# Kernel tuning notes

Hardware: AMD Instinct MI355X
Metric: run time of the kernel (lower is better)

The kernel has to match this reference:

```python
import jax, jax.numpy as jnp
import numpy as np

B, T, E, D = 8, 2048, 1024, 128  # batch, seq (== block_size), n_embedding, head size


def setup_inputs() -> dict:
    key = jax.random.key(0)
    kx, kk, kq, kv = jax.random.split(key, 4)
    scale_w = E ** -0.5  # ~torch Linear init scale
    return {
        "x": jax.random.normal(kx, (B, T, E), dtype=jnp.float32),
        "Wk": jax.random.normal(kk, (E, D), dtype=jnp.float32) * scale_w,
        "Wq": jax.random.normal(kq, (E, D), dtype=jnp.float32) * scale_w,
        "Wv": jax.random.normal(kv, (E, D), dtype=jnp.float32) * scale_w,
    }


def reference(x, Wk, Wq, Wv):
    # Training path of SelfAttentionHead.forward (use_cache=False).
    k = x @ Wk  # [B,T,D]
    q = x @ Wq  # [B,T,D]
    v = x @ Wv  # [B,T,D]
    Tlen = x.shape[1]
    scores = jnp.einsum("btd,bsd->bts", q, k) * (Wk.shape[1] ** -0.5)  # [B,T,T]
    causal = jnp.tril(jnp.ones((Tlen, Tlen), dtype=bool))
    scores = jnp.where(causal, scores, jnp.float32(-jnp.inf))
    wei = jax.nn.softmax(scores, axis=-1)
    out = jnp.einsum("bts,bsd->btd", wei, v)  # [B,T,D]
    return out
```

## Files before the change

### kernel.cpp

```cpp
#include <hip/hip_runtime.h>
#include <hip/hip_bf16.h>
#include <stdint.h>

#define Bq 8
#define Tq 2048
#define Eq 1024
#define Dq 128
#define BLOCKS_PER_B 144
#define NBLK (Bq * BLOCKS_PER_B)

typedef __attribute__((ext_vector_type(8))) short short8;
typedef __attribute__((ext_vector_type(4))) float f32x4;

__device__ __forceinline__ unsigned short f2b(float f) {
  __hip_bfloat16 h = __float2bfloat16(f);
  return __builtin_bit_cast(unsigned short, h);
}
__device__ __forceinline__ float b2f(unsigned short u) {
  unsigned int x = ((unsigned int)u) << 16;
  return __builtin_bit_cast(float, x);
}
__device__ __forceinline__ void gload16(const void* g, void* l) {
  __builtin_amdgcn_global_load_lds(
      (const __attribute__((address_space(1))) unsigned int*)g,
      (__attribute__((address_space(3))) unsigned int*)l, 16, 0, 0);
}

__global__ __launch_bounds__(256) void prep_w_kernel(const float* __restrict__ wq,
                                                     const float* __restrict__ wk,
                                                     const float* __restrict__ wv,
                                                     unsigned short* __restrict__ wt) {
  __shared__ float tile[64][129];
  const int p  = blockIdx.x >> 4;
  const int e0 = (blockIdx.x & 15) * 64;
  const float* w = (p == 0) ? wq : (p == 1) ? wk : wv;
  const int tid = threadIdx.x;
#pragma unroll
  for (int i = 0; i < 32; ++i) {
    int idx = i * 256 + tid;
    int r = idx >> 7, c = idx & 127;
    tile[r][c] = w[(size_t)(e0 + r) * Dq + c];
  }
  __syncthreads();
  const int d = tid >> 1;
  const int es = (tid & 1) * 32;
  unsigned short* dst = wt + (size_t)p * Dq * Eq + (size_t)d * Eq + e0 + es;
#pragma unroll
  for (int c4 = 0; c4 < 8; ++c4) {
    ushort4 u;
    u.x = f2b(tile[es + c4 * 4 + 0][d]);
    u.y = f2b(tile[es + c4 * 4 + 1][d]);
    u.z = f2b(tile[es + c4 * 4 + 2][d]);
    u.w = f2b(tile[es + c4 * 4 + 3][d]);
    *reinterpret_cast<ushort4*>(dst + c4 * 4) = u;
  }
}

__global__ __launch_bounds__(256) void proj3_kernel(const float* __restrict__ x,
                                                    const unsigned short* __restrict__ wt,
                                                    unsigned short* __restrict__ qo,
                                                    unsigned short* __restrict__ ko,
                                                    unsigned short* __restrict__ vo) {
  __shared__ __align__(16) char As[2][4096];
  __shared__ __align__(16) char Bs[3][8192];

  const int bid = blockIdx.x;
  const int L   = (bid & 7) * 96 + (bid >> 3);
  const int rt  = L / 3;
  const int p   = L - rt * 3;
  const int row0 = rt * 64;

  const int tid  = threadIdx.x;
  const int lane = tid & 63;
  const int w    = tid >> 6;
  const int wm   = w >> 1, wn = w & 1;
  const int lrow = lane & 15;
  const int lgrp = lane >> 4;
  const char* wtbyte = (const char*)wt + (size_t)p * Dq * 2048;

  const int arow8 = tid >> 3;
  const int ac16  = tid & 7;
  const float* asrc = x + (size_t)(row0 + arow8) * Eq + ac16 * 4;

  auto BSTAGE = [&](int bufi, int ks) {
#pragma unroll
    for (int i = 0; i < 2; ++i) {
      int col = i * 64 + (tid >> 2);
      int off = (tid & 3) * 16;
      gload16(wtbyte + (size_t)col * 2048 + ks * 2 + (off ^ (((col >> 1) & 3) << 4)),
              Bs[bufi] + i * 4096 + w * 1024);
    }
  };
  auto ALOAD = [&](int ks, float4& r0, float4& r1) {
    r0 = *reinterpret_cast<const float4*>(asrc + ks);
    r1 = *reinterpret_cast<const float4*>(asrc + (size_t)32 * Eq + ks);
  };
  auto AWRITE = [&](int bufi, const float4& r0, const float4& r1) {
#pragma unroll
    for (int i = 0; i < 2; ++i) {
      const float4& f = i ? r1 : r0;
      int row = i * 32 + arow8;
      int byte = row * 64 + ((ac16 * 8) ^ (((row >> 1) & 3) << 4));
      ushort4 u;
      u.x = f2b(f.x); u.y = f2b(f.y); u.z = f2b(f.z); u.w = f2b(f.w);
      *reinterpret_cast<ushort4*>(As[bufi] + byte) = u;
    }
  };

  f32x4 acc[2][4];
#pragma unroll
  for (int m = 0; m < 2; ++m)
#pragma unroll
    for (int n = 0; n < 4; ++n) acc[m][n] = (f32x4){0.f, 0.f, 0.f, 0.f};

  float4 Pa0, Pa1, Pb0, Pb1;
  ALOAD(0, Pa0, Pa1);
  BSTAGE(0, 0);
  BSTAGE(1, 32);
  AWRITE(0, Pa0, Pa1);
  ALOAD(32, Pb0, Pb1);
  asm volatile("s_waitcnt lgkmcnt(0)" ::: "memory");
  __builtin_amdgcn_sched_barrier(0);
  __builtin_amdgcn_s_barrier();

  auto STEP = [&](int t, float4& W0, float4& W1, float4& L0, float4& L1) {
    if (t < 31) {
      asm volatile("s_waitcnt vmcnt(4)" ::: "memory");
    } else {
      asm volatile("s_waitcnt vmcnt(0)" ::: "memory");
    }
    __builtin_amdgcn_sched_barrier(0);
    __builtin_amdgcn_s_barrier();

    if (t < 30) {
      ALOAD((t + 2) * 32, L0, L1);
      BSTAGE((t + 2) % 3, (t + 2) * 32);
    }

    const char* Ab = As[t & 1];
    const char* Bb = Bs[t % 3];
    short8 af[2], bf_[4];
#pragma unroll
    for (int m = 0; m < 2; ++m) {
      int ar = wm * 32 + m * 16 + lrow;
      af[m] = *reinterpret_cast<const short8*>(Ab + ar * 64 + ((lgrp * 16) ^ (((ar >> 1) & 3) << 4)));
    }
#pragma unroll
    for (int n = 0; n < 4; ++n) {
      int bc = wn * 64 + n * 16 + lrow;
      bf_[n] = *reinterpret_cast<const short8*>(Bb + bc * 64 + ((lgrp * 16) ^ (((bc >> 1) & 3) << 4)));
    }
#pragma unroll
    for (int m = 0; m < 2; ++m)
#pragma unroll
      for (int n = 0; n < 4; ++n)
        acc[m][n] = __builtin_amdgcn_mfma_f32_16x16x32_bf16(af[m], bf_[n], acc[m][n], 0, 0, 0);

    if (t < 31) AWRITE((t + 1) & 1, W0, W1);
    asm volatile("s_waitcnt lgkmcnt(0)" ::: "memory");
  };

  for (int tt = 0; tt < 32; tt += 2) {
    STEP(tt,     Pb0, Pb1, Pa0, Pa1);
    STEP(tt + 1, Pa0, Pa1, Pb0, Pb1);
  }

  const int rg   = lgrp * 4;
  const int lcol = lrow;
  if (p < 2) {
    unsigned short* out = (p == 0) ? qo : ko;
#pragma unroll
    for (int m = 0; m < 2; ++m)
#pragma unroll
      for (int n = 0; n < 4; ++n)
#pragma unroll
        for (int r = 0; r < 4; ++r)
          out[(size_t)(row0 + wm * 32 + m * 16 + rg + r) * Dq + wn * 64 + n * 16 + lcol] =
              f2b(acc[m][n][r]);
  } else {
#pragma unroll
    for (int m = 0; m < 2; ++m)
#pragma unroll
      for (int n = 0; n < 4; ++n)
#pragma unroll
        for (int r = 0; r < 4; ++r) {
          int trow = row0 + wm * 32 + m * 16 + rg + r;
          int bb = trow >> 11;
          int t  = trow & (Tq - 1);
          vo[(size_t)bb * Dq * Tq + (size_t)(wn * 64 + n * 16 + lcol) * Tq + t] = f2b(acc[m][n][r]);
        }
  }
}

__global__ __launch_bounds__(256) void attn_kernel(const unsigned short* __restrict__ q,
                                                   const unsigned short* __restrict__ k,
                                                   const unsigned short* __restrict__ vT,
                                                   unsigned short* __restrict__ pO,
                                                   float* __restrict__ pl) {
  __shared__ __align__(16) char kbuf[16384];
  __shared__ __align__(16) char vbuf[16384];
  __shared__ __align__(16) unsigned short pbuf[4][1024];

  const int lane = threadIdx.x & 63;
  const int w    = threadIdx.x >> 6;
  const int bx   = blockIdx.x;
  const int b    = bx / BLOCKS_PER_B;
  int rm = bx - b * BLOCKS_PER_B;
  int g = 0, s = 0;
#pragma unroll
  for (int c = 1; c <= 8; ++c) {
    int cnt = 4 * c;
    if (rm < cnt) { g = 4 * (c - 1) + rm / c; s = rm % c; break; }
    rm -= cnt;
  }
  const int kv0      = 256 * s;
  const int kend_blk = min(kv0 + 256, 64 * g + 64);
  const int qb0      = 64 * g + 16 * w;
  const int kend_w   = qb0 + 16;

  const int lrow = lane & 15;
  const int lgrp = lane >> 4;
  const int lk8  = lgrp * 8;
  const float kscale = 0.08838834764831845f * 1.44269504088896340736f;
  const float M0 = 8.0f;
  unsigned short* pb = pbuf[w];
  const char* kgbase = (const char*)(k + (size_t)b * Tq * Dq);
  const char* vgbase = (const char*)(vT + (size_t)b * Dq * Tq);

  short8 ones;
#pragma unroll
  for (int j = 0; j < 8; ++j) ones[j] = (short)0x3F80;

  short8 kr[4], vr[4];
  auto LOADREGS = [&](int kvb) {
    const char* ks = kgbase + (size_t)kvb * 256;
#pragma unroll
    for (int i = 0; i < 4; ++i) {
      int yl = i * 4096 + w * 1024 + lane * 16;
      kr[i] = *reinterpret_cast<const short8*>(ks + yl);
    }
#pragma unroll
    for (int i = 0; i < 4; ++i) {
      int yl = i * 4096 + w * 1024 + lane * 16;
      int d  = yl >> 7;
      vr[i] = *reinterpret_cast<const short8*>(vgbase + (size_t)d * 4096 + kvb * 2 + (yl & 127));
    }
    __builtin_amdgcn_sched_barrier(0);
  };
  auto WRITEREGS = [&]() {
#pragma unroll
    for (int i = 0; i < 4; ++i) {
      int yl = i * 4096 + w * 1024 + lane * 16;
      *reinterpret_cast<short8*>(kbuf + (yl ^ ((((yl >> 8) & 7)) << 4))) = kr[i];
    }
#pragma unroll
    for (int i = 0; i < 4; ++i) {
      int yl = i * 4096 + w * 1024 + lane * 16;
      int d  = yl >> 7;
      int dst = (yl & ~127) | ((yl & 127) ^ ((d & 7) << 4));
      *reinterpret_cast<short8*>(vbuf + dst) = vr[i];
    }
  };

  short8 qf[4];
  const unsigned short* qrow = q + ((size_t)b * Tq + qb0 + lrow) * Dq;
#pragma unroll
  for (int kc = 0; kc < 4; ++kc)
    qf[kc] = *reinterpret_cast<const short8*>(qrow + kc * 32 + lk8);

  f32x4 o[8];
#pragma unroll
  for (int n = 0; n < 8; ++n) o[n] = (f32x4){0.f, 0.f, 0.f, 0.f};
  f32x4 ol = (f32x4){0.f, 0.f, 0.f, 0.f};
  const int rowg = qb0 + lgrp * 4;

  const int nsteps = (kend_blk - kv0) >> 6;
  LOADREGS(kv0);
  asm volatile("s_waitcnt vmcnt(0)" ::: "memory");
  WRITEREGS();
  asm volatile("s_waitcnt lgkmcnt(0)" ::: "memory");
  __builtin_amdgcn_sched_barrier(0);
  __builtin_amdgcn_s_barrier();

  for (int t = 0; t < nsteps; ++t) {
    const int kvb = kv0 + (t << 6);
    if (t + 1 < nsteps) LOADREGS(kvb + 64);

    if (kvb < kend_w) {
      f32x4 sf[4];
#pragma unroll
      for (int n = 0; n < 4; ++n) sf[n] = (f32x4){0.f, 0.f, 0.f, 0.f};
#pragma unroll
      for (int kc = 0; kc < 4; ++kc)
#pragma unroll
        for (int n = 0; n < 4; ++n) {
          int u = (n * 16 + lrow) * 256 + kc * 64 + lgrp * 16;
          short8 kf = *reinterpret_cast<const short8*>(kbuf + (u ^ ((lrow & 7) << 4)));
          sf[n] = __builtin_amdgcn_mfma_f32_16x16x32_bf16(qf[kc], kf, sf[n], 0, 0, 0);
        }

      const bool needmask = (kvb + 64 > qb0);
      float p[4][4];
#pragma unroll
      for (int n = 0; n < 4; ++n)
#pragma unroll
        for (int r = 0; r < 4; ++r) {
          float aa = sf[n][r] * kscale;
          if (needmask && (kvb + n * 16 + lrow > rowg + r)) aa = -1e30f;
          p[n][r] = exp2f(aa - M0);
        }

#pragma unroll
      for (int n = 0; n < 4; ++n)
#pragma unroll
        for (int r = 0; r < 4; ++r) {
          int row = lgrp * 4 + r;
          int byte = row * 128 + (n * 16 + lrow) * 2;
          byte ^= (row & 7) << 4;
          *reinterpret_cast<unsigned short*>(reinterpret_cast<char*>(pb) + byte) = f2b(p[n][r]);
        }
      asm volatile("s_waitcnt lgkmcnt(0)" ::: "memory");
      __builtin_amdgcn_sched_barrier(0);
      int rbyte0 = (lrow * 128 + lgrp * 16) ^ ((lrow & 7) << 4);
      int rbyte1 = (lrow * 128 + 64 + lgrp * 16) ^ ((lrow & 7) << 4);
      short8 pf0 = *reinterpret_cast<const short8*>(reinterpret_cast<char*>(pb) + rbyte0);
      short8 pf1 = *reinterpret_cast<const short8*>(reinterpret_cast<char*>(pb) + rbyte1);

#pragma unroll
      for (int n = 0; n < 8; ++n) {
        int u0 = (n * 16 + lrow) * 128 + lgrp * 16;
        short8 vf0 = *reinterpret_cast<const short8*>(vbuf + (u0 ^ ((lrow & 7) << 4)));
        short8 vf1 = *reinterpret_cast<const short8*>(vbuf + ((u0 + 64) ^ ((lrow & 7) << 4)));
        o[n] = __builtin_amdgcn_mfma_f32_16x16x32_bf16(pf0, vf0, o[n], 0, 0, 0);
        o[n] = __builtin_amdgcn_mfma_f32_16x16x32_bf16(pf1, vf1, o[n], 0, 0, 0);
      }
      ol = __builtin_amdgcn_mfma_f32_16x16x32_bf16(pf0, ones, ol, 0, 0, 0);
      ol = __builtin_amdgcn_mfma_f32_16x16x32_bf16(pf1, ones, ol, 0, 0, 0);
    }
    __builtin_amdgcn_s_barrier();
    if (t + 1 < nsteps) {
      asm volatile("s_waitcnt vmcnt(0)" ::: "memory");
      WRITEREGS();
      asm volatile("s_waitcnt lgkmcnt(0)" ::: "memory");
      __builtin_amdgcn_sched_barrier(0);
    }
    __builtin_amdgcn_s_barrier();
  }

  unsigned short* po = pO + (size_t)bx * (64 * 128) + (size_t)(16 * w) * 128;
#pragma unroll
  for (int n = 0; n < 8; ++n)
#pragma unroll
    for (int r = 0; r < 4; ++r)
      po[(size_t)(lgrp * 4 + r) * 128 + n * 16 + lrow] = f2b(o[n][r]);
  if (lrow == 0) {
#pragma unroll
    for (int r = 0; r < 4; ++r)
      pl[(size_t)bx * 64 + 16 * w + lgrp * 4 + r] = ol[r];
  }
}

__global__ __launch_bounds__(256) void combine_kernel(const unsigned short* __restrict__ pO,
                                                      const float* __restrict__ pl,
                                                      float* __restrict__ out) {
  const int tile = blockIdx.x;
  const int b = tile >> 5;
  const int g = tile & 31;
  const int qq = g >> 2, rr = g & 3;
  const int nseg = qq + 1;
  const int slot0 = b * BLOCKS_PER_B + g + 2 * qq * (qq - 1) + qq * rr;

  __shared__ float fac[64];
  const int t = threadIdx.x;
  if (t < 64) {
    float L = 0.f;
    for (int s = 0; s < nseg; ++s) L += pl[(size_t)(slot0 + s) * 64 + t];
    fac[t] = 1.0f / L;
  }
  __syncthreads();

#pragma unroll
  for (int pass = 0; pass < 8; ++pass) {
    int i4 = pass * 256 + t;
    int row = i4 >> 5;
    int c4 = i4 & 31;
    float4 acc = make_float4(0.f, 0.f, 0.f, 0.f);
    for (int s = 0; s < nseg; ++s) {
      const ushort4 u = reinterpret_cast<const ushort4*>(pO + (size_t)(slot0 + s) * 8192 + row * 128)[c4];
      acc.x += b2f(u.x);
      acc.y += b2f(u.y);
      acc.z += b2f(u.z);
      acc.w += b2f(u.w);
    }
    float f = fac[row];
    acc.x *= f; acc.y *= f; acc.z *= f; acc.w *= f;
    reinterpret_cast<float4*>(out + ((size_t)b * Tq + g * 64 + row) * Dq)[c4] = acc;
  }
}

extern "C" void kernel_launch(void* const* d_in, const int* in_sizes, int n_in,
                              void* d_out, int out_size, void* d_ws, size_t ws_size,
                              hipStream_t stream) {
  const float* x  = (const float*)d_in[0];
  const float* Wk = (const float*)d_in[1];
  const float* Wq = (const float*)d_in[2];
  const float* Wv = (const float*)d_in[3];
  float* out = (float*)d_out;

  unsigned short* wt = (unsigned short*)d_ws;
  unsigned short* qb = wt + (size_t)3 * Dq * Eq;
  unsigned short* kb = qb + (size_t)Bq * Tq * Dq;
  unsigned short* vb = kb + (size_t)Bq * Tq * Dq;
  unsigned short* pO = vb + (size_t)Bq * Tq * Dq;
  float* pl = (float*)(pO + (size_t)NBLK * 64 * 128);

  prep_w_kernel<<<48, 256, 0, stream>>>(Wq, Wk, Wv, wt);
  proj3_kernel<<<768, 256, 0, stream>>>(x, wt, qb, kb, vb);
  attn_kernel<<<NBLK, 256, 0, stream>>>(qb, kb, vb, pO, pl);
  combine_kernel<<<Bq * Tq / 64, 256, 0, stream>>>(pO, pl, out);
}
```

Before: 89.58 us.

## Enlarge projection tile to 256 rows with 512-thread blocks

```diff
diff --git a/kernel.cpp b/kernel.cpp
--- a/kernel.cpp
+++ b/kernel.cpp
@@ -56,76 +56,73 @@
   }
 }
 
-__global__ __launch_bounds__(256) void proj3_kernel(const float* __restrict__ x,
+__global__ __launch_bounds__(512) void proj3_kernel(const float* __restrict__ x,
                                                     const unsigned short* __restrict__ wt,
                                                     unsigned short* __restrict__ qo,
                                                     unsigned short* __restrict__ ko,
                                                     unsigned short* __restrict__ vo) {
-  __shared__ __align__(16) char As[2][4096];
+  __shared__ __align__(16) char As[2][16384];
   __shared__ __align__(16) char Bs[3][8192];
 
   const int bid = blockIdx.x;
-  const int L   = (bid & 7) * 96 + (bid >> 3);
+  const int L   = (bid & 7) * 24 + (bid >> 3);
   const int rt  = L / 3;
   const int p   = L - rt * 3;
-  const int row0 = rt * 64;
+  const int row0 = rt * 256;
 
   const int tid  = threadIdx.x;
   const int lane = tid & 63;
-  const int w    = tid >> 6;
-  const int wm   = w >> 1, wn = w & 1;
+  const int wid  = tid >> 6;
+  const int wm   = wid >> 1, wn = wid & 1;
   const int lrow = lane & 15;
   const int lgrp = lane >> 4;
   const char* wtbyte = (const char*)wt + (size_t)p * Dq * 2048;
 
-  const int arow8 = tid >> 3;
-  const int ac16  = tid & 7;
-  const float* asrc = x + (size_t)(row0 + arow8) * Eq + ac16 * 4;
+  const int arow = tid >> 3;
+  const int ac16 = tid & 7;
+  const float* asrc = x + (size_t)(row0 + arow) * Eq + ac16 * 4;
 
   auto BSTAGE = [&](int bufi, int ks) {
-#pragma unroll
-    for (int i = 0; i < 2; ++i) {
-      int col = i * 64 + (tid >> 2);
-      int off = (tid & 3) * 16;
-      gload16(wtbyte + (size_t)col * 2048 + ks * 2 + (off ^ (((col >> 1) & 3) << 4)),
-              Bs[bufi] + i * 4096 + w * 1024);
-    }
-  };
-  auto ALOAD = [&](int ks, float4& r0, float4& r1) {
-    r0 = *reinterpret_cast<const float4*>(asrc + ks);
-    r1 = *reinterpret_cast<const float4*>(asrc + (size_t)32 * Eq + ks);
-  };
-  auto AWRITE = [&](int bufi, const float4& r0, const float4& r1) {
-#pragma unroll
-    for (int i = 0; i < 2; ++i) {
-      const float4& f = i ? r1 : r0;
-      int row = i * 32 + arow8;
+    int col = tid >> 2;
+    int off = (tid & 3) * 16;
+    gload16(wtbyte + (size_t)col * 2048 + ks * 2 + (off ^ (((col >> 1) & 3) << 4)),
+            Bs[bufi] + tid * 16);
+  };
+  auto ALOAD = [&](f32x4* P, int ks) {
+#pragma unroll
+    for (int i = 0; i < 4; ++i)
+      P[i] = *reinterpret_cast<const f32x4*>(asrc + (size_t)i * 64 * Eq + ks);
+  };
+  auto AWRITE = [&](int bufi, const f32x4* P) {
+#pragma unroll
+    for (int i = 0; i < 4; ++i) {
+      int row = arow + i * 64;
       int byte = row * 64 + ((ac16 * 8) ^ (((row >> 1) & 3) << 4));
       ushort4 u;
-      u.x = f2b(f.x); u.y = f2b(f.y); u.z = f2b(f.z); u.w = f2b(f.w);
+      u.x = f2b(P[i][0]); u.y = f2b(P[i][1]); u.z = f2b(P[i][2]); u.w = f2b(P[i][3]);
       *reinterpret_cast<ushort4*>(As[bufi] + byte) = u;
     }
   };
 
-  f32x4 acc[2][4];
-#pragma unroll
-  for (int m = 0; m < 2; ++m)
+  f32x4 acc[4][4];
+#pragma unroll
+  for (int m = 0; m < 4; ++m)
 #pragma unroll
     for (int n = 0; n < 4; ++n) acc[m][n] = (f32x4){0.f, 0.f, 0.f, 0.f};
 
-  float4 Pa0, Pa1, Pb0, Pb1;
-  ALOAD(0, Pa0, Pa1);
+  f32x4 Pa[4], Pb[4];
+  ALOAD(Pa, 0);
   BSTAGE(0, 0);
+  AWRITE(0, Pa);
+  ALOAD(Pb, 32);
   BSTAGE(1, 32);
-  AWRITE(0, Pa0, Pa1);
-  ALOAD(32, Pb0, Pb1);
   asm volatile("s_waitcnt lgkmcnt(0)" ::: "memory");
   __builtin_amdgcn_sched_barrier(0);
   __builtin_amdgcn_s_barrier();
 
-  auto STEP = [&](int t, float4& W0, float4& W1, float4& L0, float4& L1) {
+  auto STEP = [&](int t, f32x4* W, f32x4* Ld) {
     if (t < 31) {
-      asm volatile("s_waitcnt vmcnt(4)" ::: "memory");
+      asm volatile("s_waitcnt vmcnt(5)" ::: "memory");
     } else {
       asm volatile("s_waitcnt vmcnt(0)" ::: "memory");
     }
@@ -133,16 +130,16 @@
     __builtin_amdgcn_s_barrier();
 
     if (t < 30) {
-      ALOAD((t + 2) * 32, L0, L1);
+      ALOAD(Ld, (t + 2) * 32);
       BSTAGE((t + 2) % 3, (t + 2) * 32);
     }
 
     const char* Ab = As[t & 1];
     const char* Bb = Bs[t % 3];
-    short8 af[2], bf_[4];
-#pragma unroll
-    for (int m = 0; m < 2; ++m) {
-      int ar = wm * 32 + m * 16 + lrow;
+    short8 af[4], bf_[4];
+#pragma unroll
+    for (int m = 0; m < 4; ++m) {
+      int ar = wm * 64 + m * 16 + lrow;
       af[m] = *reinterpret_cast<const short8*>(Ab + ar * 64 + ((lgrp * 16) ^ (((ar >> 1) & 3) << 4)));
     }
 #pragma unroll
@@ -151,18 +148,18 @@
       bf_[n] = *reinterpret_cast<const short8*>(Bb + bc * 64 + ((lgrp * 16) ^ (((bc >> 1) & 3) << 4)));
     }
 #pragma unroll
-    for (int m = 0; m < 2; ++m)
+    for (int m = 0; m < 4; ++m)
 #pragma unroll
       for (int n = 0; n < 4; ++n)
         acc[m][n] = __builtin_amdgcn_mfma_f32_16x16x32_bf16(af[m], bf_[n], acc[m][n], 0, 0, 0);
 
-    if (t < 31) AWRITE((t + 1) & 1, W0, W1);
+    if (t < 31) AWRITE((t + 1) & 1, W);
     asm volatile("s_waitcnt lgkmcnt(0)" ::: "memory");
   };
 
   for (int tt = 0; tt < 32; tt += 2) {
-    STEP(tt,     Pb0, Pb1, Pa0, Pa1);
-    STEP(tt + 1, Pa0, Pa1, Pb0, Pb1);
+    STEP(tt,     Pb, Pa);
+    STEP(tt + 1, Pa, Pb);
   }
 
   const int rg   = lgrp * 4;
@@ -170,21 +167,21 @@
   if (p < 2) {
     unsigned short* out = (p == 0) ? qo : ko;
 #pragma unroll
-    for (int m = 0; m < 2; ++m)
+    for (int m = 0; m < 4; ++m)
 #pragma unroll
       for (int n = 0; n < 4; ++n)
 #pragma unroll
         for (int r = 0; r < 4; ++r)
-          out[(size_t)(row0 + wm * 32 + m * 16 + rg + r) * Dq + wn * 64 + n * 16 + lcol] =
+          out[(size_t)(row0 + wm * 64 + m * 16 + rg + r) * Dq + wn * 64 + n * 16 + lcol] =
               f2b(acc[m][n][r]);
   } else {
 #pragma unroll
-    for (int m = 0; m < 2; ++m)
+    for (int m = 0; m < 4; ++m)
 #pragma unroll
       for (int n = 0; n < 4; ++n)
 #pragma unroll
         for (int r = 0; r < 4; ++r) {
-          int trow = row0 + wm * 32 + m * 16 + rg + r;
+          int trow = row0 + wm * 64 + m * 16 + rg + r;
           int bb = trow >> 11;
           int t  = trow & (Tq - 1);
           vo[(size_t)bb * Dq * Tq + (size_t)(wn * 64 + n * 16 + lcol) * Tq + t] = f2b(acc[m][n][r]);
@@ -415,7 +412,7 @@
   float* pl = (float*)(pO + (size_t)NBLK * 64 * 128);
 
   prep_w_kernel<<<48, 256, 0, stream>>>(Wq, Wk, Wv, wt);
-  proj3_kernel<<<768, 256, 0, stream>>>(x, wt, qb, kb, vb);
+  proj3_kernel<<<192, 512, 0, stream>>>(x, wt, qb, kb, vb);
   attn_kernel<<<NBLK, 256, 0, stream>>>(qb, kb, vb, pO, pl);
   combine_kernel<<<Bq * Tq / 64, 256, 0, stream>>>(pO, pl, out);
 }
```

Result: slower. 101.7 us (+13.5%).

## Double query rows per wave to reuse K/V tiles across 128-row blocks

Applied to the files above, without the earlier changes.

```diff
diff --git a/kernel.cpp b/kernel.cpp
--- a/kernel.cpp
+++ b/kernel.cpp
@@ -6,7 +6,7 @@
 #define Tq 2048
 #define Eq 1024
 #define Dq 128
-#define BLOCKS_PER_B 144
+#define BLOCKS_PER_B 72
 #define NBLK (Bq * BLOCKS_PER_B)
 
 typedef __attribute__((ext_vector_type(8))) short short8;
@@ -199,24 +199,24 @@
                                                    float* __restrict__ pl) {
   __shared__ __align__(16) char kbuf[16384];
   __shared__ __align__(16) char vbuf[16384];
-  __shared__ __align__(16) unsigned short pbuf[4][1024];
+  __shared__ __align__(16) unsigned short pbuf[4][2048];
 
   const int lane = threadIdx.x & 63;
   const int w    = threadIdx.x >> 6;
   const int bx   = blockIdx.x;
   const int b    = bx / BLOCKS_PER_B;
   int rm = bx - b * BLOCKS_PER_B;
-  int g = 0, s = 0;
+  int G = 0, s = 0;
 #pragma unroll
   for (int c = 1; c <= 8; ++c) {
-    int cnt = 4 * c;
-    if (rm < cnt) { g = 4 * (c - 1) + rm / c; s = rm % c; break; }
+    int cnt = 2 * c;
+    if (rm < cnt) { G = 2 * (c - 1) + rm / c; s = rm % c; break; }
     rm -= cnt;
   }
   const int kv0      = 256 * s;
-  const int kend_blk = min(kv0 + 256, 64 * g + 64);
-  const int qb0      = 64 * g + 16 * w;
-  const int kend_w   = qb0 + 16;
+  const int kend_blk = min(kv0 + 256, 128 * G + 128);
+  const int qb0      = 128 * G + 32 * w;
+  const int kend_w   = qb0 + 32;
 
   const int lrow = lane & 15;
   const int lgrp = lane >> 4;
@@ -262,17 +262,23 @@
     }
   };
 
-  short8 qf[4];
-  const unsigned short* qrow = q + ((size_t)b * Tq + qb0 + lrow) * Dq;
-#pragma unroll
-  for (int kc = 0; kc < 4; ++kc)
-    qf[kc] = *reinterpret_cast<const short8*>(qrow + kc * 32 + lk8);
-
-  f32x4 o[8];
-#pragma unroll
-  for (int n = 0; n < 8; ++n) o[n] = (f32x4){0.f, 0.f, 0.f, 0.f};
-  f32x4 ol = (f32x4){0.f, 0.f, 0.f, 0.f};
-  const int rowg = qb0 + lgrp * 4;
+  short8 qf[2][4];
+#pragma unroll
+  for (int rs = 0; rs < 2; ++rs) {
+    const unsigned short* qrow = q + ((size_t)b * Tq + qb0 + rs * 16 + lrow) * Dq;
+#pragma unroll
+    for (int kc = 0; kc < 4; ++kc)
+      qf[rs][kc] = *reinterpret_cast<const short8*>(qrow + kc * 32 + lk8);
+  }
+
+  f32x4 o[2][8];
+#pragma unroll
+  for (int rs = 0; rs < 2; ++rs)
+#pragma unroll
+    for (int n = 0; n < 8; ++n) o[rs][n] = (f32x4){0.f, 0.f, 0.f, 0.f};
+  f32x4 ol[2];
+  ol[0] = (f32x4){0.f, 0.f, 0.f, 0.f};
+  ol[1] = (f32x4){0.f, 0.f, 0.f, 0.f};
 
   const int nsteps = (kend_blk - kv0) >> 6;
   LOADREGS(kv0);
@@ -287,55 +293,64 @@
     if (t + 1 < nsteps) LOADREGS(kvb + 64);
 
     if (kvb < kend_w) {
-      f32x4 sf[4];
-#pragma unroll
-      for (int n = 0; n < 4; ++n) sf[n] = (f32x4){0.f, 0.f, 0.f, 0.f};
+      f32x4 sf[2][4];
+#pragma unroll
+      for (int rs = 0; rs < 2; ++rs)
+#pragma unroll
+        for (int n = 0; n < 4; ++n) sf[rs][n] = (f32x4){0.f, 0.f, 0.f, 0.f};
 #pragma unroll
       for (int kc = 0; kc < 4; ++kc)
 #pragma unroll
         for (int n = 0; n < 4; ++n) {
           int u = (n * 16 + lrow) * 256 + kc * 64 + lgrp * 16;
           short8 kf = *reinterpret_cast<const short8*>(kbuf + (u ^ ((lrow & 7) << 4)));
-          sf[n] = __builtin_amdgcn_mfma_f32_16x16x32_bf16(qf[kc], kf, sf[n], 0, 0, 0);
+          sf[0][n] = __builtin_amdgcn_mfma_f32_16x16x32_bf16(qf[0][kc], kf, sf[0][n], 0, 0, 0);
+          sf[1][n] = __builtin_amdgcn_mfma_f32_16x16x32_bf16(qf[1][kc], kf, sf[1][n], 0, 0, 0);
         }
 
-      const bool needmask = (kvb + 64 > qb0);
-      float p[4][4];
-#pragma unroll
-      for (int n = 0; n < 4; ++n)
-#pragma unroll
-        for (int r = 0; r < 4; ++r) {
-          float aa = sf[n][r] * kscale;
-          if (needmask && (kvb + n * 16 + lrow > rowg + r)) aa = -1e30f;
-          p[n][r] = exp2f(aa - M0);
-        }
-
-#pragma unroll
-      for (int n = 0; n < 4; ++n)
-#pragma unroll
-        for (int r = 0; r < 4; ++r) {
-          int row = lgrp * 4 + r;
-          int byte = row * 128 + (n * 16 + lrow) * 2;
-          byte ^= (row & 7) << 4;
-          *reinterpret_cast<unsigned short*>(reinterpret_cast<char*>(pb) + byte) = f2b(p[n][r]);
-        }
+#pragma unroll
+      for (int rs = 0; rs < 2; ++rs) {
+        const int rowg = qb0 + rs * 16 + lgrp * 4;
+        const bool needmask = (kvb + 64 > qb0 + rs * 16);
+#pragma unroll
+        for (int n = 0; n < 4; ++n)
+#pragma unroll
+          for (int r = 0; r < 4; ++r) {
+            float aa = sf[rs][n][r] * kscale;
+            if (needmask && (kvb + n * 16 + lrow > rowg + r)) aa = -1e30f;
+            float pv = exp2f(aa - M0);
+            int row = lgrp * 4 + r;
+            int byte = rs * 2048 + ((row * 128 + (n * 16 + lrow) * 2) ^ ((row & 7) << 4));
+            *reinterpret_cast<unsigned short*>(reinterpret_cast<char*>(pb) + byte) = f2b(pv);
+          }
+      }
       asm volatile("s_waitcnt lgkmcnt(0)" ::: "memory");
       __builtin_amdgcn_sched_barrier(0);
-      int rbyte0 = (lrow * 128 + lgrp * 16) ^ ((lrow & 7) << 4);
-      int rbyte1 = (lrow * 128 + 64 + lgrp * 16) ^ ((lrow & 7) << 4);
-      short8 pf0 = *reinterpret_cast<const short8*>(reinterpret_cast<char*>(pb) + rbyte0);
-      short8 pf1 = *reinterpret_cast<const short8*>(reinterpret_cast<char*>(pb) + rbyte1);
+      short8 pf[2][2];
+#pragma unroll
+      for (int rs = 0; rs < 2; ++rs) {
+        int rbyte0 = rs * 2048 + ((lrow * 128 + lgrp * 16) ^ ((lrow & 7) << 4));
+        int rbyte1 = rs * 2048 + ((lrow * 128 + 64 + lgrp * 16) ^ ((lrow & 7) << 4));
+        pf[rs][0] = *reinterpret_cast<const short8*>(reinterpret_cast<char*>(pb) + rbyte0);
+        pf[rs][1] = *reinterpret_cast<const short8*>(reinterpret_cast<char*>(pb) + rbyte1);
+      }
 
 #pragma unroll
       for (int n = 0; n < 8; ++n) {
         int u0 = (n * 16 + lrow) * 128 + lgrp * 16;
         short8 vf0 = *reinterpret_cast<const short8*>(vbuf + (u0 ^ ((lrow & 7) << 4)));
         short8 vf1 = *reinterpret_cast<const short8*>(vbuf + ((u0 + 64) ^ ((lrow & 7) << 4)));
-        o[n] = __builtin_amdgcn_mfma_f32_16x16x32_bf16(pf0, vf0, o[n], 0, 0, 0);
-        o[n] = __builtin_amdgcn_mfma_f32_16x16x32_bf16(pf1, vf1, o[n], 0, 0, 0);
+#pragma unroll
+        for (int rs = 0; rs < 2; ++rs) {
+          o[rs][n] = __builtin_amdgcn_mfma_f32_16x16x32_bf16(pf[rs][0], vf0, o[rs][n], 0, 0, 0);
+          o[rs][n] = __builtin_amdgcn_mfma_f32_16x16x32_bf16(pf[rs][1], vf1, o[rs][n], 0, 0, 0);
+        }
       }
-      ol = __builtin_amdgcn_mfma_f32_16x16x32_bf16(pf0, ones, ol, 0, 0, 0);
-      ol = __builtin_amdgcn_mfma_f32_16x16x32_bf16(pf1, ones, ol, 0, 0, 0);
+#pragma unroll
+      for (int rs = 0; rs < 2; ++rs) {
+        ol[rs] = __builtin_amdgcn_mfma_f32_16x16x32_bf16(pf[rs][0], ones, ol[rs], 0, 0, 0);
+        ol[rs] = __builtin_amdgcn_mfma_f32_16x16x32_bf16(pf[rs][1], ones, ol[rs], 0, 0, 0);
+      }
     }
     __builtin_amdgcn_s_barrier();
     if (t + 1 < nsteps) {
@@ -347,16 +362,20 @@
     __builtin_amdgcn_s_barrier();
   }
 
-  unsigned short* po = pO + (size_t)bx * (64 * 128) + (size_t)(16 * w) * 128;
-#pragma unroll
-  for (int n = 0; n < 8; ++n)
-#pragma unroll
-    for (int r = 0; r < 4; ++r)
-      po[(size_t)(lgrp * 4 + r) * 128 + n * 16 + lrow] = f2b(o[n][r]);
+  unsigned short* po = pO + (size_t)bx * (128 * 128) + (size_t)(32 * w) * 128;
+#pragma unroll
+  for (int rs = 0; rs < 2; ++rs)
+#pragma unroll
+    for (int n = 0; n < 8; ++n)
+#pragma unroll
+      for (int r = 0; r < 4; ++r)
+        po[(size_t)(rs * 16 + lgrp * 4 + r) * 128 + n * 16 + lrow] = f2b(o[rs][n][r]);
   if (lrow == 0) {
 #pragma unroll
-    for (int r = 0; r < 4; ++r)
-      pl[(size_t)bx * 64 + 16 * w + lgrp * 4 + r] = ol[r];
+    for (int rs = 0; rs < 2; ++rs)
+#pragma unroll
+      for (int r = 0; r < 4; ++r)
+        pl[(size_t)bx * 128 + 32 * w + rs * 16 + lgrp * 4 + r] = ol[rs][r];
   }
 }
 
@@ -364,29 +383,30 @@
                                                       const float* __restrict__ pl,
                                                       float* __restrict__ out) {
   const int tile = blockIdx.x;
-  const int b = tile >> 5;
-  const int g = tile & 31;
-  const int qq = g >> 2, rr = g & 3;
-  const int nseg = qq + 1;
-  const int slot0 = b * BLOCKS_PER_B + g + 2 * qq * (qq - 1) + qq * rr;
-
-  __shared__ float fac[64];
+  const int b = tile >> 4;
+  const int G = tile & 15;
+  const int m = G >> 1;
+  const int off = (G & 1) ? (m + 1) * (m + 1) : m * (m + 1);
+  const int nseg = (G + 2) >> 1;
+  const int slot0 = b * BLOCKS_PER_B + off;
+
+  __shared__ float fac[128];
   const int t = threadIdx.x;
-  if (t < 64) {
+  if (t < 128) {
     float L = 0.f;
-    for (int s = 0; s < nseg; ++s) L += pl[(size_t)(slot0 + s) * 64 + t];
+    for (int s = 0; s < nseg; ++s) L += pl[(size_t)(slot0 + s) * 128 + t];
     fac[t] = 1.0f / L;
   }
   __syncthreads();
 
 #pragma unroll
-  for (int pass = 0; pass < 8; ++pass) {
+  for (int pass = 0; pass < 16; ++pass) {
     int i4 = pass * 256 + t;
     int row = i4 >> 5;
     int c4 = i4 & 31;
     float4 acc = make_float4(0.f, 0.f, 0.f, 0.f);
     for (int s = 0; s < nseg; ++s) {
-      const ushort4 u = reinterpret_cast<const ushort4*>(pO + (size_t)(slot0 + s) * 8192 + row * 128)[c4];
+      const ushort4 u = reinterpret_cast<const ushort4*>(pO + (size_t)(slot0 + s) * 16384 + row * 128)[c4];
       acc.x += b2f(u.x);
       acc.y += b2f(u.y);
       acc.z += b2f(u.z);
@@ -394,7 +414,7 @@
     }
     float f = fac[row];
     acc.x *= f; acc.y *= f; acc.z *= f; acc.w *= f;
-    reinterpret_cast<float4*>(out + ((size_t)b * Tq + g * 64 + row) * Dq)[c4] = acc;
+    reinterpret_cast<float4*>(out + ((size_t)b * Tq + G * 128 + row) * Dq)[c4] = acc;
   }
 }
 
@@ -412,10 +432,10 @@
   unsigned short* kb = qb + (size_t)Bq * Tq * Dq;
   unsigned short* vb = kb + (size_t)Bq * Tq * Dq;
   unsigned short* pO = vb + (size_t)Bq * Tq * Dq;
-  float* pl = (float*)(pO + (size_t)NBLK * 64 * 128);
+  float* pl = (float*)(pO + (size_t)NBLK * 128 * 128);
 
   prep_w_kernel<<<48, 256, 0, stream>>>(Wq, Wk, Wv, wt);
   proj3_kernel<<<768, 256, 0, stream>>>(x, wt, qb, kb, vb);
   attn_kernel<<<NBLK, 256, 0, stream>>>(qb, kb, vb, pO, pl);
-  combine_kernel<<<Bq * Tq / 64, 256, 0, stream>>>(pO, pl, out);
-}
+  combine_kernel<<<Bq * Tq / 128, 256, 0, stream>>>(pO, pl, out);
+}
```

Measured after the change: 123.4 us. 37.8% more time.
